# Kernel optimization log

Hardware: AMD Instinct MI355X
Metric: run time of the kernel (lower is better)

## Reference

```python
import jax, jax.numpy as jnp
import numpy as np

N_NODES = 100000
N_EDGES = 1600000
IN_F, HID, OUT_F = 256, 128, 48
ALPHA = 0.01
K = 10
# SparseDropout with dropout_prob=0 keeps all edges but scales by 1/(1-0+1e-5)
DROP_SCALE = 1.0 / (1.0 + 1e-5)


def setup_inputs() -> dict:
    key = jax.random.key(0)
    ks = jax.random.split(key, 8)
    x = jax.random.normal(ks[0], (N_NODES, IN_F), dtype=jnp.float32)
    rows = jax.random.randint(ks[1], (N_EDGES,), 0, N_NODES, dtype=jnp.int32)
    cols = jax.random.randint(ks[2], (N_EDGES,), 0, N_NODES, dtype=jnp.int32)
    vals = jax.random.uniform(ks[3], (N_EDGES,), dtype=jnp.float32)
    # Linear params (Kaiming-uniform-ish like torch defaults)
    lim1 = 1.0 / np.sqrt(IN_F)
    W1 = jax.random.uniform(ks[4], (IN_F, HID), minval=-lim1, maxval=lim1, dtype=jnp.float32)
    b1 = jax.random.uniform(ks[5], (HID,), minval=-lim1, maxval=lim1, dtype=jnp.float32)
    lim2 = 1.0 / np.sqrt(HID)
    W2 = jax.random.uniform(ks[6], (HID, OUT_F), minval=-lim2, maxval=lim2, dtype=jnp.float32)
    b2 = jax.random.uniform(ks[7], (OUT_F,), minval=-lim2, maxval=lim2, dtype=jnp.float32)
    return {"x": x, "rows": rows, "cols": cols, "vals": vals,
            "W1": W1, "b1": b1, "W2": W2, "b2": b2}


def reference(x, rows, cols, vals, W1, b1, W2, b2):
    # MLP (dropout=0 -> identity)
    h = jax.nn.relu(x @ W1 + b1)          # [N, HID]
    h = h @ W2 + b2                        # [N, OUT_F]
    v = vals * DROP_SCALE                  # SparseDropout(p=0) value scaling
    # K-step APPNP propagation: h <- (1-alpha) * A @ h + alpha * h
    def step(h, _):
        ah = jax.ops.segment_sum(v[:, None] * h[cols], rows, num_segments=N_NODES)
        return (1.0 - ALPHA) * ah + ALPHA * h, None
    h, _ = jax.lax.scan(step, h, None, length=K)
    return h
```

## Files before the change

### kernel.cpp

```cpp
#include <hip/hip_runtime.h>

#define N_NODES 100000
#define N_EDGES 1600000
#define IN_F 256
#define HID 128
#define OUT_F 48
#define PAD_F 64
#define ALPHA 0.01f
#define K_STEPS 10
#define DROP_SCALE (1.0f / (1.0f + 1e-5f))

#define NBUCK 196
#define BCAP 10240
#define EPB 4096
#define ROW_MASK_CLR 0xFFFFFFFFFC01FFFFULL

#define XCONV_BLOCKS 6250
#define CONVW_BLOCKS 153
#define BUCKET_BLOCKS 391

typedef __bf16 v8bf __attribute__((ext_vector_type(8)));
typedef float v4f __attribute__((ext_vector_type(4)));
typedef unsigned long long u64;

static __device__ __forceinline__ __bf16 tobf(float f) { return (__bf16)f; }
static __device__ __forceinline__ unsigned pack2(float a, float b) {
  unsigned short lo = __builtin_bit_cast(unsigned short, (__bf16)a);
  unsigned short hi = __builtin_bit_cast(unsigned short, (__bf16)b);
  return ((unsigned)hi << 16) | lo;
}

__global__ __launch_bounds__(256) void fused_pre(
    const float* __restrict__ x, const float* __restrict__ W1,
    const float* __restrict__ W2, __bf16* __restrict__ xb,
    __bf16* __restrict__ w1t, __bf16* __restrict__ w2t,
    const int* __restrict__ rows, const int* __restrict__ cols,
    const float* __restrict__ vals, int* __restrict__ bcur,
    u64* __restrict__ brec) {
  __shared__ int lhist[NBUCK];
  __shared__ int lbase[NBUCK];
  const int tid = threadIdx.x;

  if (blockIdx.x < XCONV_BLOCKS) {
    int c = blockIdx.x * 256 + tid;
    const float4* xp = (const float4*)(x + (size_t)c * 16);
    float4 f0 = xp[0], f1 = xp[1], f2 = xp[2], f3 = xp[3];
    uint4 o0 = make_uint4(pack2(f0.x, f0.y), pack2(f0.z, f0.w),
                          pack2(f1.x, f1.y), pack2(f1.z, f1.w));
    uint4 o1 = make_uint4(pack2(f2.x, f2.y), pack2(f2.z, f2.w),
                          pack2(f3.x, f3.y), pack2(f3.z, f3.w));
    uint4* op = (uint4*)(xb + (size_t)c * 16);
    op[0] = o0;
    op[1] = o1;
  } else if (blockIdx.x < XCONV_BLOCKS + CONVW_BLOCKS) {
    int i = (blockIdx.x - XCONV_BLOCKS) * 256 + tid;
    if (i < HID * IN_F) {
      int n = i >> 8, k = i & 255;
      w1t[i] = tobf(W1[k * HID + n]);
    }
    int j = i - HID * IN_F;
    if (j >= 0 && j < OUT_F * HID) {
      int n = j >> 7, k = j & 127;
      w2t[j] = tobf(W2[k * OUT_F + n]);
    }
  } else {
    const int bid = blockIdx.x - XCONV_BLOCKS - CONVW_BLOCKS;
    const int base = bid * EPB;

    for (int i = tid; i < NBUCK; i += 256) lhist[i] = 0;
    __syncthreads();

    u64 rec[16];
    short bb[16];
    short pp[16];
#pragma unroll
    for (int j = 0; j < 4; j++) {
      int e = base + j * 1024 + tid * 4;
      bool ok = e < N_EDGES;
      int4 r4 = ok ? *(const int4*)(rows + e) : make_int4(0, 0, 0, 0);
      int4 c4 = ok ? *(const int4*)(cols + e) : make_int4(0, 0, 0, 0);
      float4 v4 = ok ? *(const float4*)(vals + e) : make_float4(0, 0, 0, 0);
      int rr[4] = {r4.x, r4.y, r4.z, r4.w};
      int cc[4] = {c4.x, c4.y, c4.z, c4.w};
      float vv[4] = {v4.x, v4.y, v4.z, v4.w};
#pragma unroll
      for (int q = 0; q < 4; q++) {
        int idx = j * 4 + q;
        int b = rr[q] >> 9;
        float v = vv[q] * (DROP_SCALE * (1.0f - ALPHA));
        rec[idx] = ((u64)__float_as_uint(v) << 32) |
                   ((u64)(rr[q] & 511) << 17) | (unsigned)cc[q];
        bb[idx] = ok ? (short)b : (short)-1;
        pp[idx] = ok ? (short)atomicAdd(&lhist[b], 1) : (short)0;
      }
    }
    __syncthreads();

    for (int i = tid; i < NBUCK; i += 256) {
      int n = lhist[i];
      lbase[i] = (n > 0) ? atomicAdd(&bcur[i * 16], n) : 0;
    }
    __syncthreads();

#pragma unroll
    for (int j = 0; j < 16; j++) {
      if (bb[j] >= 0)
        brec[(size_t)bb[j] * BCAP + lbase[bb[j]] + pp[j]] = rec[j];
    }
  }
}

__global__ __launch_bounds__(256, 4) void mlp_mfma(
    const __bf16* __restrict__ xb, const __bf16* __restrict__ w1t,
    const float* __restrict__ b1, const __bf16* __restrict__ w2t,
    const float* __restrict__ b2, __bf16* __restrict__ h0) {
  __shared__ __bf16 h1s[64][136];

  const int tid = threadIdx.x;
  const int wv = tid >> 6;
  const int l = tid & 63;
  const int lm = l & 15;
  const int ko = (l >> 4) * 8;
  const int gw = blockIdx.x * 4 + wv;
  if (gw >= N_NODES / 16) return;
  const int n0w = gw * 16;
  const int xrow = n0w + lm;

  const __bf16* xbr = xb + (size_t)xrow * IN_F + ko;
  v8bf a8[8];
#pragma unroll
  for (int k0 = 0; k0 < 8; k0++) a8[k0] = *(const v8bf*)(xbr + k0 * 32);

  v4f acc1[8];
#pragma unroll
  for (int nf = 0; nf < 8; nf++) acc1[nf] = (v4f){0.f, 0.f, 0.f, 0.f};

#pragma unroll
  for (int k0 = 0; k0 < 8; k0++) {
    const __bf16* w1base = w1t + (size_t)lm * IN_F + k0 * 32 + ko;
#pragma unroll
    for (int nf = 0; nf < 8; nf++) {
      v8bf b = *(const v8bf*)(w1base + nf * 16 * IN_F);
      acc1[nf] = __builtin_amdgcn_mfma_f32_16x16x32_bf16(a8[k0], b, acc1[nf], 0, 0, 0);
    }
  }

#pragma unroll
  for (int nf = 0; nf < 8; nf++) {
    float bb = b1[nf * 16 + lm];
#pragma unroll
    for (int q = 0; q < 4; q++) {
      int rr = (wv << 4) + (l >> 4) * 4 + q;
      h1s[rr][nf * 16 + lm] = tobf(fmaxf(acc1[nf][q] + bb, 0.f));
    }
  }
  __syncthreads();

  const int lrow = (wv << 4) + lm;
  v4f acc2[3];
#pragma unroll
  for (int nf = 0; nf < 3; nf++) acc2[nf] = (v4f){0.f, 0.f, 0.f, 0.f};
  const __bf16* w2base = w2t + (size_t)lm * HID + ko;
#pragma unroll
  for (int k0 = 0; k0 < 4; k0++) {
    v8bf a = *(const v8bf*)&h1s[lrow][k0 * 32 + ko];
#pragma unroll
    for (int nf = 0; nf < 3; nf++) {
      v8bf b = *(const v8bf*)(w2base + nf * 16 * HID + k0 * 32);
      acc2[nf] = __builtin_amdgcn_mfma_f32_16x16x32_bf16(a, b, acc2[nf], 0, 0, 0);
    }
  }
#pragma unroll
  for (int nf = 0; nf < 3; nf++) {
    float bb = b2[nf * 16 + lm];
#pragma unroll
    for (int q = 0; q < 4; q++) {
      int node = n0w + (l >> 4) * 4 + q;
      h0[(size_t)node * PAD_F + nf * 16 + lm] = tobf(acc2[nf][q] + bb);
    }
  }
  if (l < 32) {
    uint4 z = make_uint4(0, 0, 0, 0);
    *(uint4*)(h0 + (size_t)(n0w + (l >> 1)) * PAD_F + 48 + (l & 1) * 8) = z;
  }
}

__global__ __launch_bounds__(256) void bscan_kernel(const int* __restrict__ bcur,
                                                    int* __restrict__ bstart,
                                                    int* __restrict__ rowptr) {
  __shared__ int s[256];
  int t = threadIdx.x;
  int v = (t < NBUCK) ? bcur[t * 16] : 0;
  s[t] = v;
  __syncthreads();
  for (int off = 1; off < 256; off <<= 1) {
    int add = (t >= off) ? s[t - off] : 0;
    __syncthreads();
    s[t] += add;
    __syncthreads();
  }
  if (t < NBUCK) bstart[t] = s[t] - v;
  if (t == 0) rowptr[N_NODES] = N_EDGES;
}

__global__ __launch_bounds__(512) void csr_kernel(
    const int* __restrict__ bcur, const int* __restrict__ bstart,
    const u64* __restrict__ brec, int* __restrict__ rowptr,
    u64* __restrict__ edges) {
  __shared__ int cnt[512];
  __shared__ int sc[512];
  const int b = blockIdx.x;
  const int t = threadIdx.x;
  const int n = bcur[b * 16];
  const int base = bstart[b];
  const size_t boff = (size_t)b * BCAP;

  cnt[t] = 0;
  __syncthreads();
  for (int i = t; i < n; i += 512)
    atomicAdd(&cnt[(int)((brec[boff + i] >> 17) & 511)], 1);
  __syncthreads();

  int v = cnt[t];
  sc[t] = v;
  __syncthreads();
  for (int off = 1; off < 512; off <<= 1) {
    int add = (t >= off) ? sc[t - off] : 0;
    __syncthreads();
    sc[t] += add;
    __syncthreads();
  }
  int excl = sc[t] - v;
  int grow = b * 512 + t;
  if (grow < N_NODES) rowptr[grow] = base + excl;
  cnt[t] = excl;
  __syncthreads();

  for (int i = t; i < n; i += 512) {
    u64 rec = brec[boff + i];
    int rr = (int)((rec >> 17) & 511);
    int p = atomicAdd(&cnt[rr], 1);
    edges[base + p] = rec & ROW_MASK_CLR;
  }
}

template <int FINAL>
__global__ __launch_bounds__(256) void prop_kernel(
    const __bf16* __restrict__ hin, __bf16* __restrict__ hout,
    float* __restrict__ fout, const int* __restrict__ rowptr,
    const u64* __restrict__ edges) {
  int wid = (blockIdx.x * 256 + threadIdx.x) >> 6;
  int lane = threadIdx.x & 63;
  if (wid >= N_NODES) return;
  const int g = lane >> 3;
  const int t = lane & 7;
  int s = __builtin_amdgcn_readfirstlane(rowptr[wid]);
  int e = __builtin_amdgcn_readfirstlane(rowptr[wid + 1]);

  float acc[8];
#pragma unroll
  for (int j = 0; j < 8; j++) acc[j] = 0.f;

  if (g == 0) {
    uint4 q = *(const uint4*)(hin + (size_t)wid * PAD_F + t * 8);
    unsigned uu[4] = {q.x, q.y, q.z, q.w};
#pragma unroll
    for (int k = 0; k < 4; k++) {
      acc[2 * k] = ALPHA * __uint_as_float(uu[k] << 16);
      acc[2 * k + 1] = ALPHA * __uint_as_float(uu[k] & 0xffff0000u);
    }
  }

  int i = s + g;
  for (; i + 8 < e; i += 16) {
    u64 r0 = edges[i];
    u64 r1 = edges[i + 8];
    int c0 = (int)(r0 & 0xffffffffu);
    int c1 = (int)(r1 & 0xffffffffu);
    float v0 = __uint_as_float((unsigned)(r0 >> 32));
    float v1 = __uint_as_float((unsigned)(r1 >> 32));
    uint4 q0 = *(const uint4*)(hin + (size_t)c0 * PAD_F + t * 8);
    uint4 q1 = *(const uint4*)(hin + (size_t)c1 * PAD_F + t * 8);
    unsigned a0[4] = {q0.x, q0.y, q0.z, q0.w};
    unsigned a1[4] = {q1.x, q1.y, q1.z, q1.w};
#pragma unroll
    for (int k = 0; k < 4; k++) {
      acc[2 * k] = fmaf(v0, __uint_as_float(a0[k] << 16), acc[2 * k]);
      acc[2 * k + 1] = fmaf(v0, __uint_as_float(a0[k] & 0xffff0000u), acc[2 * k + 1]);
    }
#pragma unroll
    for (int k = 0; k < 4; k++) {
      acc[2 * k] = fmaf(v1, __uint_as_float(a1[k] << 16), acc[2 * k]);
      acc[2 * k + 1] = fmaf(v1, __uint_as_float(a1[k] & 0xffff0000u), acc[2 * k + 1]);
    }
  }
  if (i < e) {
    u64 r0 = edges[i];
    int c0 = (int)(r0 & 0xffffffffu);
    float v0 = __uint_as_float((unsigned)(r0 >> 32));
    uint4 q0 = *(const uint4*)(hin + (size_t)c0 * PAD_F + t * 8);
    unsigned a0[4] = {q0.x, q0.y, q0.z, q0.w};
#pragma unroll
    for (int k = 0; k < 4; k++) {
      acc[2 * k] = fmaf(v0, __uint_as_float(a0[k] << 16), acc[2 * k]);
      acc[2 * k + 1] = fmaf(v0, __uint_as_float(a0[k] & 0xffff0000u), acc[2 * k + 1]);
    }
  }

#pragma unroll
  for (int m = 8; m <= 32; m <<= 1) {
#pragma unroll
    for (int j = 0; j < 8; j++) acc[j] += __shfl_xor(acc[j], m, 64);
  }

  if (g == 0) {
    if (FINAL) {
      if (t < 6) {
        float* dst = fout + (size_t)wid * OUT_F + t * 8;
        v4f lo4 = {acc[0], acc[1], acc[2], acc[3]};
        v4f hi4 = {acc[4], acc[5], acc[6], acc[7]};
        __builtin_nontemporal_store(lo4, (v4f*)dst);
        __builtin_nontemporal_store(hi4, (v4f*)(dst + 4));
      }
    } else {
      unsigned w[4];
#pragma unroll
      for (int k = 0; k < 4; k++) {
        unsigned short lo = __builtin_bit_cast(unsigned short, (__bf16)acc[2 * k]);
        unsigned short hi = __builtin_bit_cast(unsigned short, (__bf16)acc[2 * k + 1]);
        w[k] = ((unsigned)hi << 16) | lo;
      }
      *(uint4*)(hout + (size_t)wid * PAD_F + t * 8) =
          make_uint4(w[0], w[1], w[2], w[3]);
    }
  }
}

extern "C" void kernel_launch(void* const* d_in, const int* in_sizes, int n_in,
                              void* d_out, int out_size, void* d_ws,
                              size_t ws_size, hipStream_t stream) {
  const float* x = (const float*)d_in[0];
  const int* rows = (const int*)d_in[1];
  const int* cols = (const int*)d_in[2];
  const float* vals = (const float*)d_in[3];
  const float* W1 = (const float*)d_in[4];
  const float* b1 = (const float*)d_in[5];
  const float* W2 = (const float*)d_in[6];
  const float* b2 = (const float*)d_in[7];
  float* out = (float*)d_out;

  char* ws = (char*)d_ws;
  const size_t XB_OFF = 0;
  const size_t HB_OFF = 0;
  const size_t EDGES_OFF = 12800000;
  const size_t HA_OFF = 51200000;
  const size_t BREC_OFF = 64000000;
  const size_t ROWPTR_OFF = 80056320;
  const size_t BCUR_OFF = 80456448;
  const size_t BSTART_OFF = 80469248;
  const size_t W1T_OFF = 80470272;
  const size_t W2T_OFF = 80535808;

  __bf16* xb = (__bf16*)(ws + XB_OFF);
  __bf16* hA = (__bf16*)(ws + HA_OFF);
  __bf16* hB = (__bf16*)(ws + HB_OFF);
  u64* edges = (u64*)(ws + EDGES_OFF);
  u64* brec = (u64*)(ws + BREC_OFF);
  int* rowptr = (int*)(ws + ROWPTR_OFF);
  int* bcur = (int*)(ws + BCUR_OFF);
  int* bstart = (int*)(ws + BSTART_OFF);
  __bf16* w1t = (__bf16*)(ws + W1T_OFF);
  __bf16* w2t = (__bf16*)(ws + W2T_OFF);

  (void)hipMemsetAsync(bcur, 0, NBUCK * 64, stream);

  fused_pre<<<XCONV_BLOCKS + CONVW_BLOCKS + BUCKET_BLOCKS, 256, 0, stream>>>(
      x, W1, W2, xb, w1t, w2t, rows, cols, vals, bcur, brec);

  mlp_mfma<<<(N_NODES / 16 + 3) / 4, 256, 0, stream>>>(xb, w1t, b1, w2t, b2, hA);

  bscan_kernel<<<1, 256, 0, stream>>>(bcur, bstart, rowptr);
  csr_kernel<<<NBUCK, 512, 0, stream>>>(bcur, bstart, brec, rowptr, edges);

  const int PROP_BLOCKS = (N_NODES * 64 + 255) / 256;
  for (int k = 0; k < K_STEPS - 1; k++) {
    const __bf16* hin = (k & 1) ? hB : hA;
    __bf16* hout = (k & 1) ? hA : hB;
    prop_kernel<0><<<PROP_BLOCKS, 256, 0, stream>>>(hin, hout, nullptr, rowptr,
                                                    edges);
  }
  prop_kernel<1><<<PROP_BLOCKS, 256, 0, stream>>>(hB, nullptr, out, rowptr,
                                                  edges);
}
```

Baseline: 550.4 us.

## Fuse MLP, bucket scan and CSR build into one heterogeneous kernel

Merges the MLP MFMA kernel, the single-block bucket scan and the CSR construction kernel into one launch, with blocks split by index between MLP work and CSR work. Each CSR block recomputes the bucket prefix scan locally instead of relying on a separate scan kernel. MLP blocks now handle 128 nodes and stage W1/W2 in LDS rather than reading them from global memory per wave. Workspace offsets move so the edges array no longer overlaps xb, which the MLP blocks still read while CSR blocks write edges. The costs are higher LDS use per block, which caps occupancy, and redundant scan work in every CSR block.

```diff
diff --git a/kernel.cpp b/kernel.cpp
--- a/kernel.cpp
+++ b/kernel.cpp
@@ -18,6 +18,8 @@
 #define XCONV_BLOCKS 6250
 #define CONVW_BLOCKS 153
 #define BUCKET_BLOCKS 391
+
+#define MLP2_BLOCKS 782
 
 typedef __bf16 v8bf __attribute__((ext_vector_type(8)));
 typedef float v4f __attribute__((ext_vector_type(4)));
@@ -110,137 +112,142 @@
   }
 }
 
-__global__ __launch_bounds__(256, 4) void mlp_mfma(
+__global__ __launch_bounds__(512, 2) void fused_mlp_csr(
     const __bf16* __restrict__ xb, const __bf16* __restrict__ w1t,
     const float* __restrict__ b1, const __bf16* __restrict__ w2t,
-    const float* __restrict__ b2, __bf16* __restrict__ h0) {
-  __shared__ __bf16 h1s[64][136];
-
-  const int tid = threadIdx.x;
-  const int wv = tid >> 6;
-  const int l = tid & 63;
-  const int lm = l & 15;
-  const int ko = (l >> 4) * 8;
-  const int gw = blockIdx.x * 4 + wv;
-  if (gw >= N_NODES / 16) return;
-  const int n0w = gw * 16;
-  const int xrow = n0w + lm;
-
-  const __bf16* xbr = xb + (size_t)xrow * IN_F + ko;
-  v8bf a8[8];
-#pragma unroll
-  for (int k0 = 0; k0 < 8; k0++) a8[k0] = *(const v8bf*)(xbr + k0 * 32);
-
-  v4f acc1[8];
-#pragma unroll
-  for (int nf = 0; nf < 8; nf++) acc1[nf] = (v4f){0.f, 0.f, 0.f, 0.f};
-
-#pragma unroll
-  for (int k0 = 0; k0 < 8; k0++) {
-    const __bf16* w1base = w1t + (size_t)lm * IN_F + k0 * 32 + ko;
-#pragma unroll
-    for (int nf = 0; nf < 8; nf++) {
-      v8bf b = *(const v8bf*)(w1base + nf * 16 * IN_F);
-      acc1[nf] = __builtin_amdgcn_mfma_f32_16x16x32_bf16(a8[k0], b, acc1[nf], 0, 0, 0);
-    }
-  }
-
-#pragma unroll
-  for (int nf = 0; nf < 8; nf++) {
-    float bb = b1[nf * 16 + lm];
-#pragma unroll
-    for (int q = 0; q < 4; q++) {
-      int rr = (wv << 4) + (l >> 4) * 4 + q;
-      h1s[rr][nf * 16 + lm] = tobf(fmaxf(acc1[nf][q] + bb, 0.f));
-    }
-  }
-  __syncthreads();
-
-  const int lrow = (wv << 4) + lm;
-  v4f acc2[3];
-#pragma unroll
-  for (int nf = 0; nf < 3; nf++) acc2[nf] = (v4f){0.f, 0.f, 0.f, 0.f};
-  const __bf16* w2base = w2t + (size_t)lm * HID + ko;
-#pragma unroll
-  for (int k0 = 0; k0 < 4; k0++) {
-    v8bf a = *(const v8bf*)&h1s[lrow][k0 * 32 + ko];
-#pragma unroll
-    for (int nf = 0; nf < 3; nf++) {
-      v8bf b = *(const v8bf*)(w2base + nf * 16 * HID + k0 * 32);
-      acc2[nf] = __builtin_amdgcn_mfma_f32_16x16x32_bf16(a, b, acc2[nf], 0, 0, 0);
-    }
-  }
-#pragma unroll
-  for (int nf = 0; nf < 3; nf++) {
-    float bb = b2[nf * 16 + lm];
-#pragma unroll
-    for (int q = 0; q < 4; q++) {
-      int node = n0w + (l >> 4) * 4 + q;
-      h0[(size_t)node * PAD_F + nf * 16 + lm] = tobf(acc2[nf][q] + bb);
-    }
-  }
-  if (l < 32) {
-    uint4 z = make_uint4(0, 0, 0, 0);
-    *(uint4*)(h0 + (size_t)(n0w + (l >> 1)) * PAD_F + 48 + (l & 1) * 8) = z;
-  }
-}
-
-__global__ __launch_bounds__(256) void bscan_kernel(const int* __restrict__ bcur,
-                                                    int* __restrict__ bstart,
-                                                    int* __restrict__ rowptr) {
-  __shared__ int s[256];
-  int t = threadIdx.x;
-  int v = (t < NBUCK) ? bcur[t * 16] : 0;
-  s[t] = v;
-  __syncthreads();
-  for (int off = 1; off < 256; off <<= 1) {
-    int add = (t >= off) ? s[t - off] : 0;
-    __syncthreads();
-    s[t] += add;
-    __syncthreads();
-  }
-  if (t < NBUCK) bstart[t] = s[t] - v;
-  if (t == 0) rowptr[N_NODES] = N_EDGES;
-}
-
-__global__ __launch_bounds__(512) void csr_kernel(
-    const int* __restrict__ bcur, const int* __restrict__ bstart,
+    const float* __restrict__ b2, __bf16* __restrict__ h0,
+    const int* __restrict__ bcur, const int* __restrict__ bstart_unused,
     const u64* __restrict__ brec, int* __restrict__ rowptr,
     u64* __restrict__ edges) {
+  __shared__ __bf16 w1s[128][264];
+  __shared__ __bf16 h1s[128][136];
+  __shared__ __bf16 w2s[48][136];
+  __shared__ int bs[256];
   __shared__ int cnt[512];
   __shared__ int sc[512];
-  const int b = blockIdx.x;
-  const int t = threadIdx.x;
-  const int n = bcur[b * 16];
-  const int base = bstart[b];
-  const size_t boff = (size_t)b * BCAP;
-
-  cnt[t] = 0;
-  __syncthreads();
-  for (int i = t; i < n; i += 512)
-    atomicAdd(&cnt[(int)((brec[boff + i] >> 17) & 511)], 1);
-  __syncthreads();
-
-  int v = cnt[t];
-  sc[t] = v;
-  __syncthreads();
-  for (int off = 1; off < 512; off <<= 1) {
-    int add = (t >= off) ? sc[t - off] : 0;
-    __syncthreads();
-    sc[t] += add;
-    __syncthreads();
-  }
-  int excl = sc[t] - v;
-  int grow = b * 512 + t;
-  if (grow < N_NODES) rowptr[grow] = base + excl;
-  cnt[t] = excl;
-  __syncthreads();
-
-  for (int i = t; i < n; i += 512) {
-    u64 rec = brec[boff + i];
-    int rr = (int)((rec >> 17) & 511);
-    int p = atomicAdd(&cnt[rr], 1);
-    edges[base + p] = rec & ROW_MASK_CLR;
+
+  const int tid = threadIdx.x;
+
+  if (blockIdx.x < MLP2_BLOCKS) {
+    const int wv = tid >> 6;
+    const int l = tid & 63;
+    const int lm = l & 15;
+    const int ko = (l >> 4) * 8;
+    const int n0 = blockIdx.x * 128;
+    const int nw = n0 + wv * 16;
+    const int xrow = nw + lm;
+
+    const __bf16* xbr = xb + (size_t)xrow * IN_F + ko;
+    v8bf a8[8];
+#pragma unroll
+    for (int k0 = 0; k0 < 8; k0++) a8[k0] = *(const v8bf*)(xbr + k0 * 32);
+
+    const uint4* w1src = (const uint4*)w1t;
+    for (int i = tid; i < 4096; i += 512)
+      *(uint4*)&w1s[i >> 5][(i & 31) * 8] = w1src[i];
+    const uint4* w2src = (const uint4*)w2t;
+    for (int i = tid; i < 768; i += 512)
+      *(uint4*)&w2s[i >> 4][(i & 15) * 8] = w2src[i];
+    __syncthreads();
+
+    v4f acc1[8];
+#pragma unroll
+    for (int nf = 0; nf < 8; nf++) acc1[nf] = (v4f){0.f, 0.f, 0.f, 0.f};
+#pragma unroll
+    for (int k0 = 0; k0 < 8; k0++) {
+#pragma unroll
+      for (int nf = 0; nf < 8; nf++) {
+        v8bf b = *(const v8bf*)&w1s[nf * 16 + lm][k0 * 32 + ko];
+        acc1[nf] = __builtin_amdgcn_mfma_f32_16x16x32_bf16(a8[k0], b, acc1[nf], 0, 0, 0);
+      }
+    }
+
+#pragma unroll
+    for (int nf = 0; nf < 8; nf++) {
+      float bb = b1[nf * 16 + lm];
+#pragma unroll
+      for (int q = 0; q < 4; q++) {
+        int rr = wv * 16 + (l >> 4) * 4 + q;
+        h1s[rr][nf * 16 + lm] = tobf(fmaxf(acc1[nf][q] + bb, 0.f));
+      }
+    }
+    __syncthreads();
+
+    const int lrow = wv * 16 + lm;
+    v4f acc2[3];
+#pragma unroll
+    for (int nf = 0; nf < 3; nf++) acc2[nf] = (v4f){0.f, 0.f, 0.f, 0.f};
+#pragma unroll
+    for (int k0 = 0; k0 < 4; k0++) {
+      v8bf a = *(const v8bf*)&h1s[lrow][k0 * 32 + ko];
+#pragma unroll
+      for (int nf = 0; nf < 3; nf++) {
+        v8bf b = *(const v8bf*)&w2s[nf * 16 + lm][k0 * 32 + ko];
+        acc2[nf] = __builtin_amdgcn_mfma_f32_16x16x32_bf16(a, b, acc2[nf], 0, 0, 0);
+      }
+    }
+#pragma unroll
+    for (int nf = 0; nf < 3; nf++) {
+      float bb = b2[nf * 16 + lm];
+#pragma unroll
+      for (int q = 0; q < 4; q++) {
+        int node = nw + (l >> 4) * 4 + q;
+        if (node < N_NODES)
+          h0[(size_t)node * PAD_F + nf * 16 + lm] = tobf(acc2[nf][q] + bb);
+      }
+    }
+    {
+      int row = tid >> 2, chunk = tid & 3;
+      int node = n0 + row;
+      if (node < N_NODES) {
+        uint2 z = make_uint2(0, 0);
+        *(uint2*)(h0 + (size_t)node * PAD_F + 48 + chunk * 4) = z;
+      }
+    }
+  } else {
+    const int b = blockIdx.x - MLP2_BLOCKS;
+    const int t = tid;
+
+    if (t < 256) bs[t] = (t < NBUCK) ? bcur[t * 16] : 0;
+    __syncthreads();
+    for (int off = 1; off < 256; off <<= 1) {
+      int add = (t < 256 && t >= off) ? bs[t - off] : 0;
+      __syncthreads();
+      if (t < 256) bs[t] += add;
+      __syncthreads();
+    }
+    const int n = bcur[b * 16];
+    const int base = bs[b] - n;
+    const size_t boff = (size_t)b * BCAP;
+    if (b == 0 && t == 0) rowptr[N_NODES] = N_EDGES;
+
+    cnt[t] = 0;
+    __syncthreads();
+    for (int i = t; i < n; i += 512)
+      atomicAdd(&cnt[(int)((brec[boff + i] >> 17) & 511)], 1);
+    __syncthreads();
+
+    int v = cnt[t];
+    sc[t] = v;
+    __syncthreads();
+    for (int off = 1; off < 512; off <<= 1) {
+      int add = (t >= off) ? sc[t - off] : 0;
+      __syncthreads();
+      sc[t] += add;
+      __syncthreads();
+    }
+    int excl = sc[t] - v;
+    int grow = b * 512 + t;
+    if (grow < N_NODES) rowptr[grow] = base + excl;
+    cnt[t] = excl;
+    __syncthreads();
+
+    for (int i = t; i < n; i += 512) {
+      u64 rec = brec[boff + i];
+      int rr = (int)((rec >> 17) & 511);
+      int p = atomicAdd(&cnt[rr], 1);
+      edges[base + p] = rec & ROW_MASK_CLR;
+    }
   }
 }
 
@@ -352,14 +359,14 @@
   char* ws = (char*)d_ws;
   const size_t XB_OFF = 0;
   const size_t HB_OFF = 0;
-  const size_t EDGES_OFF = 12800000;
   const size_t HA_OFF = 51200000;
-  const size_t BREC_OFF = 64000000;
-  const size_t ROWPTR_OFF = 80056320;
-  const size_t BCUR_OFF = 80456448;
-  const size_t BSTART_OFF = 80469248;
-  const size_t W1T_OFF = 80470272;
-  const size_t W2T_OFF = 80535808;
+  const size_t EDGES_OFF = 64000000;
+  const size_t BREC_OFF = 76800000;
+  const size_t ROWPTR_OFF = 92856320;
+  const size_t BCUR_OFF = 93256448;
+  const size_t BSTART_OFF = 93268992;
+  const size_t W1T_OFF = 93270016;
+  const size_t W2T_OFF = 93335552;
 
   __bf16* xb = (__bf16*)(ws + XB_OFF);
   __bf16* hA = (__bf16*)(ws + HA_OFF);
@@ -377,10 +384,8 @@
   fused_pre<<<XCONV_BLOCKS + CONVW_BLOCKS + BUCKET_BLOCKS, 256, 0, stream>>>(
       x, W1, W2, xb, w1t, w2t, rows, cols, vals, bcur, brec);
 
-  mlp_mfma<<<(N_NODES / 16 + 3) / 4, 256, 0, stream>>>(xb, w1t, b1, w2t, b2, hA);
-
-  bscan_kernel<<<1, 256, 0, stream>>>(bcur, bstart, rowptr);
-  csr_kernel<<<NBUCK, 512, 0, stream>>>(bcur, bstart, brec, rowptr, edges);
+  fused_mlp_csr<<<MLP2_BLOCKS + NBUCK, 512, 0, stream>>>(
+      xb, w1t, b1, w2t, b2, hA, bcur, bstart, brec, rowptr, edges);
 
   const int PROP_BLOCKS = (N_NODES * 64 + 255) / 256;
   for (int k = 0; k < K_STEPS - 1; k++) {
```

Measured after the change: 508.1 us. 7.7% less time.
